# Optimization experiments

Measured on AMD Instinct MI355X. Metric: run time of the kernel, lower is better.

## Reference

```python
import jax, jax.numpy as jnp
import numpy as np

N_NODES = 100000
N_EDGES = 1000000
IN_CH = 128
OUT_CH = 128
T_DIM = 64


def setup_inputs() -> dict:
    key = jax.random.key(0)
    ks = jax.random.split(key, 9)
    x = jax.random.normal(ks[0], (N_NODES, IN_CH), dtype=jnp.float32)
    edge_index = jax.random.randint(ks[1], (2, N_EDGES), 0, N_NODES, dtype=jnp.int64)
    temporal_features = jax.random.normal(ks[2], (N_EDGES, T_DIM), dtype=jnp.float32)
    # Learned params (torch nn.Linear convention: weight [out, in], bias [out])
    s = 1.0 / np.sqrt(IN_CH)
    st = 1.0 / np.sqrt(T_DIM)
    W_S_w = jax.random.uniform(ks[3], (OUT_CH, IN_CH), minval=-s, maxval=s, dtype=jnp.float32)
    W_S_b = jax.random.uniform(ks[4], (OUT_CH,), minval=-s, maxval=s, dtype=jnp.float32)
    W_T_w = jax.random.uniform(ks[5], (OUT_CH, IN_CH), minval=-s, maxval=s, dtype=jnp.float32)
    W_T_b = jax.random.uniform(ks[6], (OUT_CH,), minval=-s, maxval=s, dtype=jnp.float32)
    T_w = jax.random.uniform(ks[7], (OUT_CH, T_DIM), minval=-st, maxval=st, dtype=jnp.float32)
    T_b = jax.random.uniform(ks[8], (OUT_CH,), minval=-st, maxval=st, dtype=jnp.float32)
    return {
        "x": x, "edge_index": edge_index, "temporal_features": temporal_features,
        "W_S_w": W_S_w, "W_S_b": W_S_b, "W_T_w": W_T_w, "W_T_b": W_T_b,
        "T_w": T_w, "T_b": T_b,
    }


def reference(x, edge_index, temporal_features, W_S_w, W_S_b, W_T_w, W_T_b, T_w, T_b):
    num_nodes = x.shape[0]
    row, col = edge_index[0], edge_index[1]
    # self transform: [N, out]
    self_features = x @ W_S_w.T + W_S_b
    # gather neighbor feats then transform: [E, out]
    neighbor_features = x[col] @ W_T_w.T + W_T_b
    # temporal encodings: [E, out]
    temporal_encodings = temporal_features @ T_w.T + T_b
    messages = neighbor_features + temporal_encodings
    # scatter-add aggregation over destination nodes
    aggregated = jax.ops.segment_sum(messages, row, num_segments=num_nodes)
    return jax.nn.relu(self_features + aggregated)
```

## Files before the change

### kernel.cpp

```cpp
#include <hip/hip_runtime.h>

#define N_NODES 100000
#define N_EDGES 1000000
#define K_TOT   320
#define NCHUNK  98

#define BM  128
#define LDA 72

typedef __attribute__((ext_vector_type(8))) short bf16x8;
typedef __attribute__((ext_vector_type(4))) float f32x4;

__device__ __forceinline__ unsigned short f2bf(float f) {
    unsigned u = __float_as_uint(f);
    u += 0x7FFFu + ((u >> 16) & 1u);
    return (unsigned short)(u >> 16);
}
__device__ __forceinline__ unsigned pack2(float a, float b) {
    return (unsigned)f2bf(a) | ((unsigned)f2bf(b) << 16);
}

__global__ void prep_kernel(const float* __restrict__ WSw,
                            const float* __restrict__ WTw,
                            const float* __restrict__ Tw,
                            const float* __restrict__ WTb,
                            const float* __restrict__ Tb,
                            unsigned short* __restrict__ Gtb,
                            float* __restrict__ bias2) {
    int idx = blockIdx.x * 256 + threadIdx.x;
    if (idx < K_TOT * 128) {
        int k = idx >> 7;
        int o = idx & 127;
        float v = (k < 128) ? WSw[o * 128 + k]
                : (k < 256) ? WTw[o * 128 + (k - 128)]
                            : Tw[o * 64 + (k - 256)];
        Gtb[(size_t)o * K_TOT + k] = f2bf(v);
    }
    if (idx < 128) bias2[idx] = WTb[idx] + Tb[idx];
}

__global__ __launch_bounds__(256) void hist_kernel(const int* __restrict__ ei,
                                                   int* __restrict__ hist) {
    int e = blockIdx.x * 256 + threadIdx.x;
    if (e < N_EDGES) atomicAdd(&hist[ei[e]], 1);
}

__global__ __launch_bounds__(256) void scan_pass1(const int* __restrict__ hist,
                                                  int* __restrict__ chunksum) {
    __shared__ int ts[256];
    int b = blockIdx.x, t = threadIdx.x;
    int i = b * 1024 + t * 4;
    int s = 0;
#pragma unroll
    for (int j = 0; j < 4; ++j)
        if (i + j < N_NODES) s += hist[i + j];
    ts[t] = s;
    __syncthreads();
    for (int off = 128; off > 0; off >>= 1) {
        if (t < off) ts[t] += ts[t + off];
        __syncthreads();
    }
    if (t == 0) chunksum[b] = ts[0];
}

__global__ void scan_mid(const int* __restrict__ chunksum,
                         int* __restrict__ chunkoff) {
    if (threadIdx.x == 0 && blockIdx.x == 0) {
        int run = 0;
        for (int i = 0; i < NCHUNK; ++i) { chunkoff[i] = run; run += chunksum[i]; }
    }
}

__global__ __launch_bounds__(256) void scan_pass2(const int* __restrict__ hist,
                                                  const int* __restrict__ chunkoff,
                                                  int* __restrict__ offsets) {
    __shared__ int ts[256];
    int b = blockIdx.x, t = threadIdx.x;
    int i0 = b * 1024 + t * 4;
    int v[4];
    int s = 0;
#pragma unroll
    for (int j = 0; j < 4; ++j) {
        v[j] = (i0 + j < N_NODES) ? hist[i0 + j] : 0;
        s += v[j];
    }
    ts[t] = s;
    __syncthreads();
    for (int off = 1; off < 256; off <<= 1) {
        int add = (t >= off) ? ts[t - off] : 0;
        __syncthreads();
        ts[t] += add;
        __syncthreads();
    }
    int run = chunkoff[b] + ts[t] - s;
#pragma unroll
    for (int j = 0; j < 4; ++j) {
        if (i0 + j < N_NODES) offsets[i0 + j] = run;
        run += v[j];
    }
    if (b == 0 && t == 0) offsets[N_NODES] = N_EDGES;
}

__global__ __launch_bounds__(256) void fill_kernel(const int* __restrict__ ei,
                                                   int* __restrict__ cursor,
                                                   unsigned long long* __restrict__ ec) {
    int e = blockIdx.x * 256 + threadIdx.x;
    if (e < N_EDGES) {
        int row = ei[e];
        int col = ei[N_EDGES + e];
        int pos = atomicAdd(&cursor[row], 1);
        ec[pos] = ((unsigned long long)(unsigned)col << 32) | (unsigned)e;
    }
}

__global__ __launch_bounds__(256) void agg_kernel(
        const float* __restrict__ x,
        const float* __restrict__ tf,
        const unsigned long long* __restrict__ ec,
        const int* __restrict__ offsets,
        float* __restrict__ aggx,
        float* __restrict__ aggt,
        float* __restrict__ deg) {
    int lane = threadIdx.x & 63;
    int n = blockIdx.x * 4 + (threadIdx.x >> 6);
    if (n >= N_NODES) return;

    int beg = offsets[n], end = offsets[n + 1];

    float ax0 = 0.f, ax1 = 0.f, at0 = 0.f;
    float bx0 = 0.f, bx1 = 0.f, bt0 = 0.f;

    int i = beg;
    for (; i + 3 < end; i += 4) {
        unsigned long long p0 = ec[i],     p1 = ec[i + 1];
        unsigned long long p2 = ec[i + 2], p3 = ec[i + 3];
        const float* x0p = x + ((size_t)(p0 >> 32) << 7);
        const float* x1p = x + ((size_t)(p1 >> 32) << 7);
        const float* x2p = x + ((size_t)(p2 >> 32) << 7);
        const float* x3p = x + ((size_t)(p3 >> 32) << 7);
        const float* t0p = tf + ((size_t)(unsigned)p0 << 6);
        const float* t1p = tf + ((size_t)(unsigned)p1 << 6);
        const float* t2p = tf + ((size_t)(unsigned)p2 << 6);
        const float* t3p = tf + ((size_t)(unsigned)p3 << 6);
        float a0 = x0p[lane], a1 = x0p[64 + lane];
        float b0 = x1p[lane], b1 = x1p[64 + lane];
        float c0 = x2p[lane], c1 = x2p[64 + lane];
        float d0 = x3p[lane], d1 = x3p[64 + lane];
        float u0 = __builtin_nontemporal_load(t0p + lane);
        float u1 = __builtin_nontemporal_load(t1p + lane);
        float u2 = __builtin_nontemporal_load(t2p + lane);
        float u3 = __builtin_nontemporal_load(t3p + lane);
        ax0 += a0; ax1 += a1; at0 += u0;
        bx0 += b0; bx1 += b1; bt0 += u1;
        ax0 += c0; ax1 += c1; at0 += u2;
        bx0 += d0; bx1 += d1; bt0 += u3;
    }
    for (; i < end; ++i) {
        unsigned long long p0 = ec[i];
        const float* xp = x + ((size_t)(p0 >> 32) << 7);
        ax0 += xp[lane];
        ax1 += xp[64 + lane];
        at0 += __builtin_nontemporal_load(tf + ((size_t)(unsigned)p0 << 6) + lane);
    }

    aggx[(size_t)n * 128 + lane]      = ax0 + bx0;
    aggx[(size_t)n * 128 + 64 + lane] = ax1 + bx1;
    aggt[(size_t)n * 64 + lane]       = at0 + bt0;
    if (lane == 0) deg[n] = (float)(end - beg);
}

__global__ __launch_bounds__(256) void gemm_kernel(
        const float* __restrict__ x,
        const float* aggx,
        const float* __restrict__ aggt,
        const unsigned short* __restrict__ Gtb,
        const float* __restrict__ WSb,
        const float* __restrict__ bias2,
        const float* __restrict__ deg,
        float* out) {
    __shared__ unsigned short As[BM * LDA];
    __shared__ unsigned short Bs[BM * LDA];

    int t = threadIdx.x;
    int lane = t & 63;
    int wave = t >> 6;
    int mw = (wave & 1) * 64;
    int nw = (wave >> 1) * 64;
    int row0 = blockIdx.x * BM;
    int quad = lane >> 4;
    int l16  = lane & 15;

    f32x4 acc[4][4];
#pragma unroll
    for (int mt = 0; mt < 4; ++mt)
#pragma unroll
        for (int nt = 0; nt < 4; ++nt)
            acc[mt][nt] = (f32x4){0.f, 0.f, 0.f, 0.f};

    int sm = t >> 1;
    int sh = (t & 1) * 32;

    for (int c = 0; c < 5; ++c) {
        const float* src; int ld, koff;
        if (c < 2)      { src = x;    ld = 128; koff = c * 64; }
        else if (c < 4) { src = aggx; ld = 128; koff = (c - 2) * 64; }
        else            { src = aggt; ld = 64;  koff = 0; }

        __syncthreads();

        int gm = row0 + sm;
        const float* ap = src + (size_t)gm * ld + koff + sh;
#pragma unroll
        for (int g = 0; g < 4; ++g) {
            float4 u0 = {0.f, 0.f, 0.f, 0.f}, u1 = u0;
            if (gm < N_NODES) {
                u0 = *(const float4*)(ap + g * 8);
                u1 = *(const float4*)(ap + g * 8 + 4);
            }
            uint4 w;
            w.x = pack2(u0.x, u0.y);
            w.y = pack2(u0.z, u0.w);
            w.z = pack2(u1.x, u1.y);
            w.w = pack2(u1.z, u1.w);
            *(uint4*)&As[sm * LDA + sh + g * 8] = w;
        }

        const unsigned short* gp = Gtb + (size_t)sm * K_TOT + c * 64 + sh;
#pragma unroll
        for (int g = 0; g < 4; ++g)
            *(uint4*)&Bs[sm * LDA + sh + g * 8] = *(const uint4*)(gp + g * 8);

        __syncthreads();

#pragma unroll
        for (int ks = 0; ks < 2; ++ks) {
            bf16x8 af[4], bfv[4];
#pragma unroll
            for (int mt = 0; mt < 4; ++mt)
                af[mt] = *(bf16x8*)&As[(mw + mt * 16 + l16) * LDA + ks * 32 + quad * 8];
#pragma unroll
            for (int nt = 0; nt < 4; ++nt)
                bfv[nt] = *(bf16x8*)&Bs[(nw + nt * 16 + l16) * LDA + ks * 32 + quad * 8];
#pragma unroll
            for (int mt = 0; mt < 4; ++mt)
#pragma unroll
                for (int nt = 0; nt < 4; ++nt)
                    acc[mt][nt] = __builtin_amdgcn_mfma_f32_16x16x32_bf16(
                        af[mt], bfv[nt], acc[mt][nt], 0, 0, 0);
        }
    }

#pragma unroll
    for (int mt = 0; mt < 4; ++mt) {
#pragma unroll
        for (int r = 0; r < 4; ++r) {
            int m = row0 + mw + mt * 16 + quad * 4 + r;
            if (m >= N_NODES) continue;
            float dg = deg[m];
#pragma unroll
            for (int nt = 0; nt < 4; ++nt) {
                int o = nw + nt * 16 + l16;
                float val = acc[mt][nt][r] + WSb[o] + dg * bias2[o];
                out[(size_t)m * 128 + o] = fmaxf(val, 0.f);
            }
        }
    }
}

extern "C" void kernel_launch(void* const* d_in, const int* in_sizes, int n_in,
                              void* d_out, int out_size, void* d_ws, size_t ws_size,
                              hipStream_t stream) {
    const float* x   = (const float*)d_in[0];
    const int*   ei  = (const int*)d_in[1];
    const float* tf  = (const float*)d_in[2];
    const float* WSw = (const float*)d_in[3];
    const float* WSb = (const float*)d_in[4];
    const float* WTw = (const float*)d_in[5];
    const float* WTb = (const float*)d_in[6];
    const float* Tw  = (const float*)d_in[7];
    const float* Tb  = (const float*)d_in[8];
    float* out = (float*)d_out;

    float* aggt  = (float*)d_ws;
    float* deg   = aggt + (size_t)N_NODES * 64;
    float* bias2 = deg + N_NODES;
    unsigned short* Gtb = (unsigned short*)(bias2 + 128);
    int* hist    = (int*)(Gtb + (size_t)K_TOT * 128);
    int* offsets = hist + N_NODES;
    int* cursor  = offsets + (N_NODES + 2);
    int* csum    = cursor + N_NODES;
    int* coff    = csum + 100;
    unsigned long long* ec = (unsigned long long*)(coff + 100);

    float* aggx = out;

    hipMemsetAsync(hist, 0, (size_t)N_NODES * sizeof(int), stream);

    prep_kernel<<<(K_TOT * 128 + 255) / 256, 256, 0, stream>>>(
        WSw, WTw, Tw, WTb, Tb, Gtb, bias2);

    hist_kernel<<<(N_EDGES + 255) / 256, 256, 0, stream>>>(ei, hist);
    scan_pass1<<<NCHUNK, 256, 0, stream>>>(hist, csum);
    scan_mid<<<1, 64, 0, stream>>>(csum, coff);
    scan_pass2<<<NCHUNK, 256, 0, stream>>>(hist, coff, offsets);

    hipMemcpyAsync(cursor, offsets, (size_t)N_NODES * sizeof(int),
                   hipMemcpyDeviceToDevice, stream);

    fill_kernel<<<(N_EDGES + 255) / 256, 256, 0, stream>>>(ei, cursor, ec);

    agg_kernel<<<N_NODES / 4, 256, 0, stream>>>(
        x, tf, ec, offsets, aggx, aggt, deg);

    gemm_kernel<<<(N_NODES + BM - 1) / BM, 256, 0, stream>>>(
        x, aggx, aggt, Gtb, WSb, bias2, deg, out);
}
```

Before: 627.0 us.

## Store GEMM operands as bf16 in workspace and drop cursor copy

The aggregation kernel now writes bf16-packed aggregates, and the prep kernel also converts x to bf16. The GEMM therefore loads half as many bytes with plain vector loads issued before the barrier, and does no in-loop conversion. The fill kernel advances the offsets array in place and the aggregation kernel reads the shifted bounds, which removes the cursor memcpy. The single-thread middle scan becomes a parallel block scan. The cost is an extra full pass over x to convert it, and padded rows past N_NODES in the workspace are read without a bounds check.

Result: faster. 599.7 us (-4.4%).

```diff
diff --git a/kernel.cpp b/kernel.cpp
--- a/kernel.cpp
+++ b/kernel.cpp
@@ -1,12 +1,15 @@
 #include <hip/hip_runtime.h>
 
 #define N_NODES 100000
+#define M_PAD   100096
 #define N_EDGES 1000000
 #define K_TOT   320
 #define NCHUNK  98
 
 #define BM  128
 #define LDA 72
+
+#define XCONV_THREADS 1600000
 
 typedef __attribute__((ext_vector_type(8))) short bf16x8;
 typedef __attribute__((ext_vector_type(4))) float f32x4;
@@ -20,23 +23,38 @@
     return (unsigned)f2bf(a) | ((unsigned)f2bf(b) << 16);
 }
 
-__global__ void prep_kernel(const float* __restrict__ WSw,
-                            const float* __restrict__ WTw,
-                            const float* __restrict__ Tw,
-                            const float* __restrict__ WTb,
-                            const float* __restrict__ Tb,
-                            unsigned short* __restrict__ Gtb,
-                            float* __restrict__ bias2) {
-    int idx = blockIdx.x * 256 + threadIdx.x;
-    if (idx < K_TOT * 128) {
-        int k = idx >> 7;
-        int o = idx & 127;
-        float v = (k < 128) ? WSw[o * 128 + k]
-                : (k < 256) ? WTw[o * 128 + (k - 128)]
-                            : Tw[o * 64 + (k - 256)];
-        Gtb[(size_t)o * K_TOT + k] = f2bf(v);
-    }
-    if (idx < 128) bias2[idx] = WTb[idx] + Tb[idx];
+__global__ __launch_bounds__(256) void prep_kernel(
+        const float* __restrict__ x,
+        const float* __restrict__ WSw,
+        const float* __restrict__ WTw,
+        const float* __restrict__ Tw,
+        const float* __restrict__ WTb,
+        const float* __restrict__ Tb,
+        unsigned short* __restrict__ xb,
+        unsigned short* __restrict__ Gtb,
+        float* __restrict__ bias2) {
+    int gid = blockIdx.x * 256 + threadIdx.x;
+    if (gid < XCONV_THREADS) {
+        const float4* p = (const float4*)x + (size_t)gid * 2;
+        float4 u0 = p[0], u1 = p[1];
+        uint4 w;
+        w.x = pack2(u0.x, u0.y);
+        w.y = pack2(u0.z, u0.w);
+        w.z = pack2(u1.x, u1.y);
+        w.w = pack2(u1.z, u1.w);
+        *(uint4*)(xb + (size_t)gid * 8) = w;
+    } else {
+        int idx = gid - XCONV_THREADS;
+        if (idx < K_TOT * 128) {
+            int k = idx >> 7;
+            int o = idx & 127;
+            float v = (k < 128) ? WSw[o * 128 + k]
+                    : (k < 256) ? WTw[o * 128 + (k - 128)]
+                                : Tw[o * 64 + (k - 256)];
+            Gtb[(size_t)o * K_TOT + k] = f2bf(v);
+        }
+        if (idx < 128) bias2[idx] = WTb[idx] + Tb[idx];
+    }
 }
 
 __global__ __launch_bounds__(256) void hist_kernel(const int* __restrict__ ei,
@@ -63,12 +81,20 @@
     if (t == 0) chunksum[b] = ts[0];
 }
 
-__global__ void scan_mid(const int* __restrict__ chunksum,
-                         int* __restrict__ chunkoff) {
-    if (threadIdx.x == 0 && blockIdx.x == 0) {
-        int run = 0;
-        for (int i = 0; i < NCHUNK; ++i) { chunkoff[i] = run; run += chunksum[i]; }
-    }
+__global__ __launch_bounds__(128) void scan_mid(const int* __restrict__ chunksum,
+                                                int* __restrict__ chunkoff) {
+    __shared__ int ts[128];
+    int t = threadIdx.x;
+    int v = (t < NCHUNK) ? chunksum[t] : 0;
+    ts[t] = v;
+    __syncthreads();
+    for (int off = 1; off < 128; off <<= 1) {
+        int a = (t >= off) ? ts[t - off] : 0;
+        __syncthreads();
+        ts[t] += a;
+        __syncthreads();
+    }
+    if (t < NCHUNK) chunkoff[t] = ts[t] - v;
 }
 
 __global__ __launch_bounds__(256) void scan_pass2(const int* __restrict__ hist,
@@ -98,17 +124,16 @@
         if (i0 + j < N_NODES) offsets[i0 + j] = run;
         run += v[j];
     }
-    if (b == 0 && t == 0) offsets[N_NODES] = N_EDGES;
 }
 
 __global__ __launch_bounds__(256) void fill_kernel(const int* __restrict__ ei,
-                                                   int* __restrict__ cursor,
+                                                   int* __restrict__ offsets,
                                                    unsigned long long* __restrict__ ec) {
     int e = blockIdx.x * 256 + threadIdx.x;
     if (e < N_EDGES) {
         int row = ei[e];
         int col = ei[N_EDGES + e];
-        int pos = atomicAdd(&cursor[row], 1);
+        int pos = atomicAdd(&offsets[row], 1);
         ec[pos] = ((unsigned long long)(unsigned)col << 32) | (unsigned)e;
     }
 }
@@ -118,66 +143,65 @@
         const float* __restrict__ tf,
         const unsigned long long* __restrict__ ec,
         const int* __restrict__ offsets,
-        float* __restrict__ aggx,
-        float* __restrict__ aggt,
+        unsigned* __restrict__ aggxb,
+        unsigned* __restrict__ aggtb,
         float* __restrict__ deg) {
     int lane = threadIdx.x & 63;
     int n = blockIdx.x * 4 + (threadIdx.x >> 6);
     if (n >= N_NODES) return;
 
-    int beg = offsets[n], end = offsets[n + 1];
-
-    float ax0 = 0.f, ax1 = 0.f, at0 = 0.f;
-    float bx0 = 0.f, bx1 = 0.f, bt0 = 0.f;
+    int beg = n ? offsets[n - 1] : 0;
+    int end = offsets[n];
+
+    float ax = 0.f, ay = 0.f, at = 0.f;
+    float bx = 0.f, by = 0.f, bt = 0.f;
 
     int i = beg;
     for (; i + 3 < end; i += 4) {
         unsigned long long p0 = ec[i],     p1 = ec[i + 1];
         unsigned long long p2 = ec[i + 2], p3 = ec[i + 3];
-        const float* x0p = x + ((size_t)(p0 >> 32) << 7);
-        const float* x1p = x + ((size_t)(p1 >> 32) << 7);
-        const float* x2p = x + ((size_t)(p2 >> 32) << 7);
-        const float* x3p = x + ((size_t)(p3 >> 32) << 7);
+        const float2* x0p = (const float2*)(x + ((size_t)(p0 >> 32) << 7)) + lane;
+        const float2* x1p = (const float2*)(x + ((size_t)(p1 >> 32) << 7)) + lane;
+        const float2* x2p = (const float2*)(x + ((size_t)(p2 >> 32) << 7)) + lane;
+        const float2* x3p = (const float2*)(x + ((size_t)(p3 >> 32) << 7)) + lane;
         const float* t0p = tf + ((size_t)(unsigned)p0 << 6);
         const float* t1p = tf + ((size_t)(unsigned)p1 << 6);
         const float* t2p = tf + ((size_t)(unsigned)p2 << 6);
         const float* t3p = tf + ((size_t)(unsigned)p3 << 6);
-        float a0 = x0p[lane], a1 = x0p[64 + lane];
-        float b0 = x1p[lane], b1 = x1p[64 + lane];
-        float c0 = x2p[lane], c1 = x2p[64 + lane];
-        float d0 = x3p[lane], d1 = x3p[64 + lane];
+        float2 a = *x0p, b = *x1p, c = *x2p, d = *x3p;
         float u0 = __builtin_nontemporal_load(t0p + lane);
         float u1 = __builtin_nontemporal_load(t1p + lane);
         float u2 = __builtin_nontemporal_load(t2p + lane);
         float u3 = __builtin_nontemporal_load(t3p + lane);
-        ax0 += a0; ax1 += a1; at0 += u0;
-        bx0 += b0; bx1 += b1; bt0 += u1;
-        ax0 += c0; ax1 += c1; at0 += u2;
-        bx0 += d0; bx1 += d1; bt0 += u3;
+        ax += a.x; ay += a.y; at += u0;
+        bx += b.x; by += b.y; bt += u1;
+        ax += c.x; ay += c.y; at += u2;
+        bx += d.x; by += d.y; bt += u3;
     }
     for (; i < end; ++i) {
         unsigned long long p0 = ec[i];
-        const float* xp = x + ((size_t)(p0 >> 32) << 7);
-        ax0 += xp[lane];
-        ax1 += xp[64 + lane];
-        at0 += __builtin_nontemporal_load(tf + ((size_t)(unsigned)p0 << 6) + lane);
-    }
-
-    aggx[(size_t)n * 128 + lane]      = ax0 + bx0;
-    aggx[(size_t)n * 128 + 64 + lane] = ax1 + bx1;
-    aggt[(size_t)n * 64 + lane]       = at0 + bt0;
+        float2 a = *((const float2*)(x + ((size_t)(p0 >> 32) << 7)) + lane);
+        ax += a.x; ay += a.y;
+        at += __builtin_nontemporal_load(tf + ((size_t)(unsigned)p0 << 6) + lane);
+    }
+
+    float fx = ax + bx, fy = ay + by, ft = at + bt;
+    aggxb[(size_t)n * 64 + lane] = pack2(fx, fy);
+    float pt = __shfl_xor(ft, 1);
+    if (!(lane & 1))
+        aggtb[(size_t)n * 32 + (lane >> 1)] = pack2(ft, pt);
     if (lane == 0) deg[n] = (float)(end - beg);
 }
 
 __global__ __launch_bounds__(256) void gemm_kernel(
-        const float* __restrict__ x,
-        const float* aggx,
-        const float* __restrict__ aggt,
+        const unsigned short* __restrict__ xb,
+        const unsigned short* __restrict__ aggxb,
+        const unsigned short* __restrict__ aggtb,
         const unsigned short* __restrict__ Gtb,
         const float* __restrict__ WSb,
         const float* __restrict__ bias2,
         const float* __restrict__ deg,
-        float* out) {
+        float* __restrict__ out) {
     __shared__ unsigned short As[BM * LDA];
     __shared__ unsigned short Bs[BM * LDA];
 
@@ -201,34 +225,32 @@
     int sh = (t & 1) * 32;
 
     for (int c = 0; c < 5; ++c) {
-        const float* src; int ld, koff;
-        if (c < 2)      { src = x;    ld = 128; koff = c * 64; }
-        else if (c < 4) { src = aggx; ld = 128; koff = (c - 2) * 64; }
-        else            { src = aggt; ld = 64;  koff = 0; }
-
-        __syncthreads();
-
-        int gm = row0 + sm;
-        const float* ap = src + (size_t)gm * ld + koff + sh;
-#pragma unroll
-        for (int g = 0; g < 4; ++g) {
-            float4 u0 = {0.f, 0.f, 0.f, 0.f}, u1 = u0;
-            if (gm < N_NODES) {
-                u0 = *(const float4*)(ap + g * 8);
-                u1 = *(const float4*)(ap + g * 8 + 4);
-            }
-            uint4 w;
-            w.x = pack2(u0.x, u0.y);
-            w.y = pack2(u0.z, u0.w);
-            w.z = pack2(u1.x, u1.y);
-            w.w = pack2(u1.z, u1.w);
-            *(uint4*)&As[sm * LDA + sh + g * 8] = w;
-        }
-
+        const unsigned short* src; int ld, koff;
+        if (c < 2)      { src = xb;    ld = 128; koff = c * 64; }
+        else if (c < 4) { src = aggxb; ld = 128; koff = (c - 2) * 64; }
+        else            { src = aggtb; ld = 64;  koff = 0; }
+
+        const unsigned short* ap = src + (size_t)(row0 + sm) * ld + koff + sh;
+        uint4 a0 = *(const uint4*)(ap);
+        uint4 a1 = *(const uint4*)(ap + 8);
+        uint4 a2 = *(const uint4*)(ap + 16);
+        uint4 a3 = *(const uint4*)(ap + 24);
         const unsigned short* gp = Gtb + (size_t)sm * K_TOT + c * 64 + sh;
-#pragma unroll
-        for (int g = 0; g < 4; ++g)
-            *(uint4*)&Bs[sm * LDA + sh + g * 8] = *(const uint4*)(gp + g * 8);
+        uint4 b0 = *(const uint4*)(gp);
+        uint4 b1 = *(const uint4*)(gp + 8);
+        uint4 b2 = *(const uint4*)(gp + 16);
+        uint4 b3 = *(const uint4*)(gp + 24);
+
+        __syncthreads();
+
+        *(uint4*)&As[sm * LDA + sh]      = a0;
+        *(uint4*)&As[sm * LDA + sh + 8]  = a1;
+        *(uint4*)&As[sm * LDA + sh + 16] = a2;
+        *(uint4*)&As[sm * LDA + sh + 24] = a3;
+        *(uint4*)&Bs[sm * LDA + sh]      = b0;
+        *(uint4*)&Bs[sm * LDA + sh + 8]  = b1;
+        *(uint4*)&Bs[sm * LDA + sh + 16] = b2;
+        *(uint4*)&Bs[sm * LDA + sh + 24] = b3;
 
         __syncthreads();
 
@@ -281,37 +303,33 @@
     const float* Tb  = (const float*)d_in[8];
     float* out = (float*)d_out;
 
-    float* aggt  = (float*)d_ws;
-    float* deg   = aggt + (size_t)N_NODES * 64;
+    unsigned short* xb    = (unsigned short*)d_ws;
+    unsigned short* aggxb = xb    + (size_t)M_PAD * 128;
+    unsigned short* aggtb = aggxb + (size_t)M_PAD * 128;
+    unsigned short* Gtb   = aggtb + (size_t)M_PAD * 64;
+    unsigned long long* ec = (unsigned long long*)(Gtb + (size_t)K_TOT * 128);
+    float* deg   = (float*)(ec + N_EDGES);
     float* bias2 = deg + N_NODES;
-    unsigned short* Gtb = (unsigned short*)(bias2 + 128);
-    int* hist    = (int*)(Gtb + (size_t)K_TOT * 128);
+    int* hist    = (int*)(bias2 + 128);
     int* offsets = hist + N_NODES;
-    int* cursor  = offsets + (N_NODES + 2);
-    int* csum    = cursor + N_NODES;
-    int* coff    = csum + 100;
-    unsigned long long* ec = (unsigned long long*)(coff + 100);
-
-    float* aggx = out;
+    int* csum    = offsets + (N_NODES + 2);
+    int* coff    = csum + 128;
 
     hipMemsetAsync(hist, 0, (size_t)N_NODES * sizeof(int), stream);
 
-    prep_kernel<<<(K_TOT * 128 + 255) / 256, 256, 0, stream>>>(
-        WSw, WTw, Tw, WTb, Tb, Gtb, bias2);
+    prep_kernel<<<(XCONV_THREADS + K_TOT * 128) / 256, 256, 0, stream>>>(
+        x, WSw, WTw, Tw, WTb, Tb, xb, Gtb, bias2);
 
     hist_kernel<<<(N_EDGES + 255) / 256, 256, 0, stream>>>(ei, hist);
     scan_pass1<<<NCHUNK, 256, 0, stream>>>(hist, csum);
-    scan_mid<<<1, 64, 0, stream>>>(csum, coff);
+    scan_mid<<<1, 128, 0, stream>>>(csum, coff);
     scan_pass2<<<NCHUNK, 256, 0, stream>>>(hist, coff, offsets);
 
-    hipMemcpyAsync(cursor, offsets, (size_t)N_NODES * sizeof(int),
-                   hipMemcpyDeviceToDevice, stream);
-
-    fill_kernel<<<(N_EDGES + 255) / 256, 256, 0, stream>>>(ei, cursor, ec);
+    fill_kernel<<<(N_EDGES + 255) / 256, 256, 0, stream>>>(ei, offsets, ec);
 
     agg_kernel<<<N_NODES / 4, 256, 0, stream>>>(
-        x, tf, ec, offsets, aggx, aggt, deg);
+        x, tf, ec, offsets, (unsigned*)aggxb, (unsigned*)aggtb, deg);
 
     gemm_kernel<<<(N_NODES + BM - 1) / BM, 256, 0, stream>>>(
-        x, aggx, aggt, Gtb, WSb, bias2, deg, out);
-}
+        xb, aggxb, aggtb, Gtb, WSb, bias2, deg, out);
+}
```
